# Kernel optimization log

Measured on AMD Instinct MI355X. Metric: run time of the kernel, lower is better.

Reference implementation:

```python
import jax, jax.numpy as jnp
import numpy as np
from functools import partial

N = 50000      # nodes
E = 800000     # edges
B = 64         # graphs in batch
D = 64         # embedding_dim (= per-head out_dim)
H = 2          # num_heads
G = 50         # n_gaussians
HID = 128      # hidden_dim of edge-filter net
MLP_DIM = 128  # mlp_dim of OutputMLP
OUT = 1        # output_dim
L = 3          # n_interactions
CUTOFF = 8.0
MEAN = 0.0
STD = 1.0


def ssp(x):
    # shifted softplus: softplus(x) - log(2)
    return jax.nn.softplus(x) - jnp.log(2.0)


def setup_inputs() -> dict:
    key = jax.random.key(0)
    ks = jax.random.split(key, 24)
    R = jax.random.normal(ks[0], (N, 3), dtype=jnp.float32) * 3.0
    Z = jax.random.randint(ks[1], (N,), 0, 100)
    src = jax.random.randint(ks[2], (E,), 0, N)
    dst = jax.random.randint(ks[3], (E,), 0, N)
    graph_ids = jnp.sort(jax.random.randint(ks[4], (N,), 0, B))
    # embedding table with padding_idx=0 zeroed
    emb_table = (jax.random.normal(ks[5], (100, D), dtype=jnp.float32) * 0.1).at[0].set(0.0)
    offsets = jnp.linspace(0.0, CUTOFF, G, dtype=jnp.float32)
    widths = jnp.full((G,), offsets[1] - offsets[0], dtype=jnp.float32)
    s = 0.1
    rn = lambda k, shp: jax.random.normal(k, shp, dtype=jnp.float32) * s
    return {
        "R": R, "Z": Z, "src": src, "dst": dst, "graph_ids": graph_ids,
        "emb_table": emb_table, "offsets": offsets, "widths": widths,
        "fc_w": rn(ks[6], (L, D, H * D)),
        "attn_l": rn(ks[7], (L, H, D)),
        "attn_r": rn(ks[8], (L, H, D)),
        "filt_w1": rn(ks[9], (L, G, HID)), "filt_b1": jnp.zeros((L, HID), jnp.float32),
        "filt_w2": rn(ks[10], (L, HID, H * D)), "filt_b2": jnp.zeros((L, H * D), jnp.float32),
        "mlp_w1": rn(ks[11], (L, H * D, D)), "mlp_b1": jnp.zeros((L, D), jnp.float32),
        "mlp_w2": rn(ks[12], (L, D, D)), "mlp_b2": jnp.zeros((L, D), jnp.float32),
        "out_w1": rn(ks[13], (D, MLP_DIM)), "out_b1": jnp.zeros((MLP_DIM,), jnp.float32),
        "out_w2": rn(ks[14], (MLP_DIM, OUT)), "out_b2": jnp.zeros((OUT,), jnp.float32),
    }


def _forward(R, emb_table, offsets, widths, fc_w, attn_l, attn_r,
             filt_w1, filt_b1, filt_w2, filt_b2,
             mlp_w1, mlp_b1, mlp_w2, mlp_b2,
             out_w1, out_b1, out_w2, out_b2,
             Z, src, dst, graph_ids):
    # per-edge distances
    r = jnp.linalg.norm(R[src] - R[dst], axis=1)  # (E,)
    # Gaussian smearing (trainable offsets/widths, schnetpack style)
    coeff = -0.5 / (widths ** 2)
    gs = jnp.exp(coeff * (r[:, None] - offsets) ** 2)  # (E, G)
    # cosine cutoff
    C = 0.5 * (jnp.cos(r * (jnp.pi / CUTOFF)) + 1.0) * (r < CUTOFF).astype(r.dtype)  # (E,)
    x = emb_table[Z]  # (N, D)
    for l in range(L):
        h = (x @ fc_w[l]).reshape(N, H, D)  # (N, H, D)
        # cfconv-style edge filter from gaussian features
        w = ssp(gs @ filt_w1[l] + filt_b1[l]) @ filt_w2[l] + filt_b2[l]  # (E, H*D)
        w = w.reshape(E, H, D)
        msg = h[src] * w * C[:, None, None]  # (E, H, D)
        # GAT attention, softmax over incoming edges per dst node
        el = jnp.einsum('nhd,hd->nh', h, attn_l[l])
        er = jnp.einsum('nhd,hd->nh', h, attn_r[l])
        e = jax.nn.leaky_relu(el[src] + er[dst], negative_slope=0.2)  # (E, H)
        m = jax.ops.segment_max(e, dst, num_segments=N)  # (N, H)
        ex = jnp.exp(e - m[dst])
        denom = jax.ops.segment_sum(ex, dst, num_segments=N)  # (N, H)
        alpha = ex / denom[dst]  # (E, H)
        agg = jax.ops.segment_sum(alpha[:, :, None] * msg, dst, num_segments=N)  # (N, H, D)
        v = ssp(agg).reshape(N, H * D)
        v = ssp(v @ mlp_w1[l] + mlp_b1[l]) @ mlp_w2[l] + mlp_b2[l]  # (N, D)
        x = x + v
    hh = ssp(x @ out_w1 + out_b1) @ out_w2 + out_b2  # (N, OUT)
    hh = hh * STD + MEAN
    return jax.ops.segment_sum(hh, graph_ids, num_segments=B)  # (B, OUT)


def reference(R, Z, src, dst, graph_ids, emb_table, offsets, widths,
              fc_w, attn_l, attn_r, filt_w1, filt_b1, filt_w2, filt_b2,
              mlp_w1, mlp_b1, mlp_w2, mlp_b2,
              out_w1, out_b1, out_w2, out_b2):
    return _forward(R, emb_table, offsets, widths, fc_w, attn_l, attn_r,
                    filt_w1, filt_b1, filt_w2, filt_b2,
                    mlp_w1, mlp_b1, mlp_w2, mlp_b2,
                    out_w1, out_b1, out_w2, out_b2,
                    Z, src, dst, graph_ids)
```

## Files before the change

### kernel.cpp

```cpp
#include <hip/hip_runtime.h>
#include <stdint.h>

#define N_NODES 50000
#define N_EDGES 800000
#define B_GRAPHS 64
#define D_DIM 64
#define HD 128
#define G_GAUSS 50
#define HID_DIM 128
#define L_LAYERS 3
#define LN2 0.69314718055994530942f
#define PI_OVER_8 0.39269908169872414f
#define NCHUNK 196

#define TN 64
#define TLD 132
#define XLD 68
#define NBLK ((N_NODES + TN - 1) / TN)

#define LUT_T 2048
#define LUT_ROWS (LUT_T + 1)
#define LROWS 8

__device__ __forceinline__ float sspf(float x) {
    float ax = fabsf(x);
    return fmaxf(x, 0.f) + __logf(1.f + __expf(-ax)) - LN2;
}
__device__ __forceinline__ unsigned short f2bf(float f) {
    union { float f; unsigned int i; } v; v.f = f;
    unsigned int u = v.i;
    return (unsigned short)((u + 0x7FFFu + ((u >> 16) & 1u)) >> 16);
}

__global__ void repr_prep(int* __restrict__ count, float* __restrict__ dout) {
    int i = blockIdx.x * 256 + threadIdx.x;
    if (i < N_NODES) count[i] = 0;
    else if (i < N_NODES + B_GRAPHS) dout[i - N_NODES] = 0.f;
}

#define NSUB (N_EDGES / 64)
#define ZB_T (2 * N_NODES / 4 + 2 * NSUB * 32)
__global__ void repr_zero_b(const int2* __restrict__ surv,
                            float* __restrict__ agg, float* __restrict__ denom) {
    int i = blockIdx.x * 256 + threadIdx.x;
    float4 z = make_float4(0.f, 0.f, 0.f, 0.f);
    if (i < 2 * N_NODES / 4) {
        ((float4*)denom)[i] = z;
    } else {
        int j = i - 2 * N_NODES / 4;
        if (j >= 2 * NSUB * 32) return;
        int row = j >> 5, c4 = j & 31;
        int sr = row >> 1;
        int p = sr * 64 + ((row & 1) ? 63 : 0);
        int d = (int)((unsigned)surv[p].x >> 16);
        *(float4*)&agg[(size_t)d * HD + c4 * 4] = z;
    }
}

__global__ __launch_bounds__(256) void repr_lut_build(
    const float* __restrict__ offs, const float* __restrict__ widths,
    const float* __restrict__ fw1, const float* __restrict__ fb1,
    const float* __restrict__ fw2, const float* __restrict__ fb2,
    unsigned int* __restrict__ lut)
{
    __shared__ float gs_s[LROWS + 1][G_GAUSS];
    __shared__ float hid_s[LROWS + 1][HID_DIM];
    __shared__ float wc_s[LROWS + 1][HD];
    const int nb = LUT_T / LROWS;
    int l = blockIdx.x / nb;
    int i0r = (blockIdx.x % nb) * LROWS;
    int tid = threadIdx.x;
    const float step = 8.0f / LUT_T;

    for (int j = tid; j < (LROWS + 1) * G_GAUSS; j += 256) {
        int r = j / G_GAUSS, k = j - r * G_GAUSS;
        float rr = (i0r + r) * step;
        float wdt = widths[k];
        float dr = rr - offs[k];
        gs_s[r][k] = expf(-0.5f / (wdt * wdt) * dr * dr);
    }
    __syncthreads();

    int c = tid & 127, sub = tid >> 7;
    int rlo = sub * 4;
    {
        const float* W1 = fw1 + (size_t)l * G_GAUSS * HID_DIM + c;
        float acc[5];
        float bb = fb1[l * HID_DIM + c];
        #pragma unroll
        for (int r = 0; r < 5; r++) acc[r] = bb;
        for (int k = 0; k < G_GAUSS; k++) {
            float wv = W1[k * HID_DIM];
            #pragma unroll
            for (int r = 0; r < 5; r++)
                acc[r] = fmaf(gs_s[rlo + r][k], wv, acc[r]);
        }
        #pragma unroll
        for (int r = 0; r < 5; r++) hid_s[rlo + r][c] = sspf(acc[r]);
    }
    __syncthreads();
    {
        const float* W2 = fw2 + (size_t)l * HID_DIM * HD + c;
        float acc[5];
        float bb = fb2[l * HD + c];
        #pragma unroll
        for (int r = 0; r < 5; r++) acc[r] = bb;
        for (int k = 0; k < HID_DIM; k++) {
            float wv = W2[k * HD];
            #pragma unroll
            for (int r = 0; r < 5; r++)
                acc[r] = fmaf(hid_s[rlo + r][k], wv, acc[r]);
        }
        #pragma unroll
        for (int r = 0; r < 5; r++) {
            float rr = (i0r + rlo + r) * step;
            float C = (rr < 8.0f) ? 0.5f * (cosf(rr * PI_OVER_8) + 1.f) : 0.f;
            wc_s[rlo + r][c] = acc[r] * C;
        }
    }
    __syncthreads();
    for (int j = tid; j < LROWS * HD; j += 256) {
        int r = j >> 7, cc = j & 127;
        unsigned int lo = f2bf(wc_s[r][cc]);
        unsigned int hi = f2bf(wc_s[r + 1][cc]);
        lut[((size_t)l * LUT_ROWS + i0r + r) * HD + cc] = lo | (hi << 16);
    }
    if (i0r == LUT_T - LROWS && tid < HD)
        lut[((size_t)l * LUT_ROWS + LUT_T) * HD + tid] = 0u;
}

__global__ void repr_hist(const float* __restrict__ R,
                          const int* __restrict__ src, const int* __restrict__ dst,
                          int* __restrict__ count,
                          int2* __restrict__ pk, unsigned short* __restrict__ rank) {
    int e = blockIdx.x * blockDim.x + threadIdx.x;
    if (e >= N_EDGES) return;
    int s = src[e], d = dst[e];
    float dx = R[3*s+0] - R[3*d+0];
    float dy = R[3*s+1] - R[3*d+1];
    float dz = R[3*s+2] - R[3*d+2];
    float r = sqrtf(dx*dx + dy*dy + dz*dz);
    unsigned rf = (r < 8.0f) ? (unsigned)(r * 16777216.f) : (2048u << 16);
    if (rf > (2048u << 16)) rf = 2048u << 16;
    pk[e] = make_int2((int)((unsigned)s | ((unsigned)d << 16)), (int)rf);
    int rnk = atomicAdd(&count[d], 1);
    rank[e] = (unsigned short)rnk;
}

__global__ void repr_scanA(const int* __restrict__ cnt, int* __restrict__ excl,
                           int* __restrict__ bsum) {
    __shared__ int tmp[256];
    int t = threadIdx.x, b = blockIdx.x;
    int i = b * 256 + t;
    int v = (i < N_NODES) ? cnt[i] : 0;
    tmp[t] = v; __syncthreads();
    for (int off = 1; off < 256; off <<= 1) {
        int add = (t >= off) ? tmp[t - off] : 0;
        __syncthreads();
        tmp[t] += add;
        __syncthreads();
    }
    if (i < N_NODES) excl[i] = tmp[t] - v;
    if (t == 255) bsum[b] = tmp[255];
}
__global__ void repr_scanB(const int* __restrict__ bsum, int* __restrict__ bpref) {
    __shared__ int tmp[256];
    int t = threadIdx.x;
    int v = (t < NCHUNK) ? bsum[t] : 0;
    tmp[t] = v; __syncthreads();
    for (int off = 1; off < 256; off <<= 1) {
        int add = (t >= off) ? tmp[t - off] : 0;
        __syncthreads();
        tmp[t] += add;
        __syncthreads();
    }
    if (t < NCHUNK) bpref[t] = tmp[t] - v;
}
__global__ void repr_scanC(const int* __restrict__ excl, const int* __restrict__ bpref,
                           int* __restrict__ rowptr) {
    int i = blockIdx.x * 256 + threadIdx.x;
    if (i < N_NODES) rowptr[i] = excl[i] + bpref[blockIdx.x];
}

__global__ void repr_scatter(const int2* __restrict__ pk,
                             const unsigned short* __restrict__ rank,
                             const int* __restrict__ rowptr,
                             int2* __restrict__ surv) {
    int e = blockIdx.x * blockDim.x + threadIdx.x;
    if (e >= N_EDGES) return;
    int2 v = pk[e];
    int d = (int)((unsigned)v.x >> 16);
    surv[rowptr[d] + (int)rank[e]] = v;
}


__device__ __forceinline__ void load_ssp_agg(int base, int tid,
        const float* __restrict__ agg, const float* __restrict__ denom,
        float* __restrict__ bufA) {
    int row = tid >> 2;
    int c0 = (tid & 3) << 5;
    int n = base + row;
    float2 dn = *(const float2*)&denom[2 * (size_t)n];
    float i0v = dn.x > 0.f ? 1.f / dn.x : 0.f;
    float i1v = dn.y > 0.f ? 1.f / dn.y : 0.f;
    float inv = (c0 < 64) ? i0v : i1v;
    const float* ap = agg + (size_t)n * HD + c0;
    float* tp = bufA + row * TLD + c0;
    #pragma unroll
    for (int j = 0; j < 8; j++) {
        float4 v = *(const float4*)(ap + j * 4);
        tp[j*4+0] = sspf(v.x * inv); tp[j*4+1] = sspf(v.y * inv);
        tp[j*4+2] = sspf(v.z * inv); tp[j*4+3] = sspf(v.w * inv);
    }
}

__device__ __forceinline__ void gemm_mlp(int base, int tid,
        const float* __restrict__ w1, const float* __restrict__ b1,
        const float* __restrict__ w2, const float* __restrict__ b2,
        float* __restrict__ x, float* __restrict__ bufA, float* __restrict__ v1s)
{
    const int rg = tid >> 4, cg = tid & 15;
    const int r0 = rg * 4, c0 = cg * 4;
    float acc[4][4];
    #pragma unroll
    for (int r = 0; r < 4; r++)
        #pragma unroll
        for (int c = 0; c < 4; c++) acc[r][c] = 0.f;
    for (int k0 = 0; k0 < 128; k0 += 4) {
        float av[4][4];
        #pragma unroll
        for (int r = 0; r < 4; r++)
            *(float4*)av[r] = *(const float4*)&bufA[(r0 + r) * TLD + k0];
        #pragma unroll
        for (int kk = 0; kk < 4; kk++) {
            float4 wv = *(const float4*)(w1 + (k0 + kk) * 64 + c0);
            float wf[4] = {wv.x, wv.y, wv.z, wv.w};
            #pragma unroll
            for (int r = 0; r < 4; r++)
                #pragma unroll
                for (int c = 0; c < 4; c++)
                    acc[r][c] = fmaf(av[r][kk], wf[c], acc[r][c]);
        }
    }
    {
        float4 bv = *(const float4*)(b1 + c0);
        float ba[4] = {bv.x, bv.y, bv.z, bv.w};
        #pragma unroll
        for (int r = 0; r < 4; r++)
            #pragma unroll
            for (int c = 0; c < 4; c++)
                v1s[(r0 + r) * XLD + c0 + c] = sspf(acc[r][c] + ba[c]);
    }
    __syncthreads();
    float acc2[4][4];
    #pragma unroll
    for (int r = 0; r < 4; r++)
        #pragma unroll
        for (int c = 0; c < 4; c++) acc2[r][c] = 0.f;
    for (int k0 = 0; k0 < 64; k0 += 4) {
        float av[4][4];
        #pragma unroll
        for (int r = 0; r < 4; r++)
            *(float4*)av[r] = *(const float4*)&v1s[(r0 + r) * XLD + k0];
        #pragma unroll
        for (int kk = 0; kk < 4; kk++) {
            float4 wv = *(const float4*)(w2 + (k0 + kk) * 64 + c0);
            float wf[4] = {wv.x, wv.y, wv.z, wv.w};
            #pragma unroll
            for (int r = 0; r < 4; r++)
                #pragma unroll
                for (int c = 0; c < 4; c++)
                    acc2[r][c] = fmaf(av[r][kk], wf[c], acc2[r][c]);
        }
    }
    {
        float4 bv = *(const float4*)(b2 + c0);
        #pragma unroll
        for (int r = 0; r < 4; r++) {
            int n = base + r0 + r;
            float4 xv = *(const float4*)(x + (size_t)n * 64 + c0);
            float4 o;
            o.x = acc2[r][0] + bv.x + xv.x;
            o.y = acc2[r][1] + bv.y + xv.y;
            o.z = acc2[r][2] + bv.z + xv.z;
            o.w = acc2[r][3] + bv.w + xv.w;
            *(float4*)&bufA[(r0 + r) * XLD + c0] = o;
            if (n < N_NODES) *(float4*)(x + (size_t)n * 64 + c0) = o;
        }
    }
    __syncthreads();
}

__device__ __forceinline__ void gemm_h(int base, int tid,
        const float* __restrict__ bufA,
        const float* __restrict__ fc_w, const float* __restrict__ attn_l,
        const float* __restrict__ attn_r,
        unsigned int* __restrict__ hq, float* __restrict__ el, float* __restrict__ er)
{
    const int rg = tid >> 4, cg = tid & 15;
    const int r0 = rg * 4, c0 = cg * 8;
    float acc[4][8];
    #pragma unroll
    for (int r = 0; r < 4; r++)
        #pragma unroll
        for (int c = 0; c < 8; c++) acc[r][c] = 0.f;
    for (int k0 = 0; k0 < 64; k0 += 4) {
        float av[4][4];
        #pragma unroll
        for (int r = 0; r < 4; r++)
            *(float4*)av[r] = *(const float4*)&bufA[(r0 + r) * XLD + k0];
        #pragma unroll
        for (int kk = 0; kk < 4; kk++) {
            float4 w0 = *(const float4*)(fc_w + (k0 + kk) * 128 + c0);
            float4 w1v = *(const float4*)(fc_w + (k0 + kk) * 128 + c0 + 4);
            float wf[8] = {w0.x, w0.y, w0.z, w0.w, w1v.x, w1v.y, w1v.z, w1v.w};
            #pragma unroll
            for (int r = 0; r < 4; r++)
                #pragma unroll
                for (int c = 0; c < 8; c++)
                    acc[r][c] = fmaf(av[r][kk], wf[c], acc[r][c]);
        }
    }
    float al[8], ar[8];
    #pragma unroll
    for (int c = 0; c < 8; c++) { al[c] = attn_l[c0 + c]; ar[c] = attn_r[c0 + c]; }
    int head = cg >> 3;
    #pragma unroll
    for (int r = 0; r < 4; r++) {
        int n = base + r0 + r;
        float pel = 0.f, per = 0.f;
        #pragma unroll
        for (int c = 0; c < 8; c++) {
            pel = fmaf(acc[r][c], al[c], pel);
            per = fmaf(acc[r][c], ar[c], per);
        }
        if (n < N_NODES) {
            uint4 pv;
            pv.x = (unsigned int)f2bf(acc[r][0]) | ((unsigned int)f2bf(acc[r][1]) << 16);
            pv.y = (unsigned int)f2bf(acc[r][2]) | ((unsigned int)f2bf(acc[r][3]) << 16);
            pv.z = (unsigned int)f2bf(acc[r][4]) | ((unsigned int)f2bf(acc[r][5]) << 16);
            pv.w = (unsigned int)f2bf(acc[r][6]) | ((unsigned int)f2bf(acc[r][7]) << 16);
            *(uint4*)(hq + (size_t)n * 64 + cg * 4) = pv;
        }
        #pragma unroll
        for (int off = 1; off < 8; off <<= 1) {
            pel += __shfl_xor(pel, off, 64);
            per += __shfl_xor(per, off, 64);
        }
        if ((cg & 7) == 0 && n < N_NODES) {
            el[n * 2 + head] = pel;
            er[n * 2 + head] = per;
        }
    }
}

__global__ __launch_bounds__(256) void repr_embed_h(
        const float* __restrict__ emb, const int* __restrict__ Z,
        const float* __restrict__ fc_w, const float* __restrict__ attn_l,
        const float* __restrict__ attn_r,
        float* __restrict__ x, unsigned int* __restrict__ hq,
        float* __restrict__ el, float* __restrict__ er) {
    __shared__ float bufA[TN * XLD];
    int base = blockIdx.x * TN, tid = threadIdx.x;
    int row = tid >> 2;
    int c0 = (tid & 3) << 4;
    int n = base + row;
    int z = (n < N_NODES) ? Z[n] : 0;
    const float* ep = emb + (size_t)z * D_DIM + c0;
    float* bp = bufA + row * XLD + c0;
    #pragma unroll
    for (int j = 0; j < 4; j++) {
        float4 v = *(const float4*)(ep + j * 4);
        *(float4*)(bp + j * 4) = v;
        if (n < N_NODES) *(float4*)(x + (size_t)n * D_DIM + c0 + j * 4) = v;
    }
    __syncthreads();
    gemm_h(base, tid, bufA, fc_w, attn_l, attn_r, hq, el, er);
}

__global__ __launch_bounds__(256) void repr_mlp_h(
        const float* __restrict__ agg, const float* __restrict__ denom,
        const float* __restrict__ w1, const float* __restrict__ b1,
        const float* __restrict__ w2, const float* __restrict__ b2,
        const float* __restrict__ fc_w, const float* __restrict__ attn_l,
        const float* __restrict__ attn_r,
        float* __restrict__ x, unsigned int* __restrict__ hq,
        float* __restrict__ el, float* __restrict__ er) {
    __shared__ float bufA[TN * TLD];
    __shared__ float v1s[TN * XLD];
    int base = blockIdx.x * TN, tid = threadIdx.x;
    load_ssp_agg(base, tid, agg, denom, bufA);
    __syncthreads();
    gemm_mlp(base, tid, w1, b1, w2, b2, x, bufA, v1s);
    gemm_h(base, tid, bufA, fc_w, attn_l, attn_r, hq, el, er);
}

__global__ __launch_bounds__(256) void repr_mlp_out(
        const float* __restrict__ agg, const float* __restrict__ denom,
        const float* __restrict__ w1, const float* __restrict__ b1,
        const float* __restrict__ w2, const float* __restrict__ b2,
        const float* __restrict__ ow1, const float* __restrict__ ob1,
        const float* __restrict__ ow2, const float* __restrict__ ob2,
        float* __restrict__ x, float* __restrict__ hh) {
    __shared__ float bufA[TN * TLD];
    __shared__ float v1s[TN * XLD];
    int base = blockIdx.x * TN, tid = threadIdx.x;
    load_ssp_agg(base, tid, agg, denom, bufA);
    __syncthreads();
    gemm_mlp(base, tid, w1, b1, w2, b2, x, bufA, v1s);
    const int rg = tid >> 4, cg = tid & 15;
    const int r0 = rg * 4, c0 = cg * 8;
    float acc[4][8];
    #pragma unroll
    for (int r = 0; r < 4; r++)
        #pragma unroll
        for (int c = 0; c < 8; c++) acc[r][c] = 0.f;
    for (int k0 = 0; k0 < 64; k0 += 4) {
        float av[4][4];
        #pragma unroll
        for (int r = 0; r < 4; r++)
            *(float4*)av[r] = *(const float4*)&bufA[(r0 + r) * XLD + k0];
        #pragma unroll
        for (int kk = 0; kk < 4; kk++) {
            float4 w0 = *(const float4*)(ow1 + (k0 + kk) * 128 + c0);
            float4 w1v = *(const float4*)(ow1 + (k0 + kk) * 128 + c0 + 4);
            float wf[8] = {w0.x, w0.y, w0.z, w0.w, w1v.x, w1v.y, w1v.z, w1v.w};
            #pragma unroll
            for (int r = 0; r < 4; r++)
                #pragma unroll
                for (int c = 0; c < 8; c++)
                    acc[r][c] = fmaf(av[r][kk], wf[c], acc[r][c]);
        }
    }
    float o1[8], w2c[8];
    #pragma unroll
    for (int c = 0; c < 8; c++) { o1[c] = ob1[c0 + c]; w2c[c] = ow2[c0 + c]; }
    #pragma unroll
    for (int r = 0; r < 4; r++) {
        int n = base + r0 + r;
        float s = 0.f;
        #pragma unroll
        for (int c = 0; c < 8; c++)
            s = fmaf(sspf(acc[r][c] + o1[c]), w2c[c], s);
        #pragma unroll
        for (int off = 1; off < 16; off <<= 1)
            s += __shfl_xor(s, off, 64);
        if (cg == 0 && n < N_NODES) hh[n] = s + ob2[0];
    }
}

#define TILE 256
__global__ __launch_bounds__(256) void repr_msg_lut(
    const int2* __restrict__ surv,
    const float* __restrict__ el, const float* __restrict__ er,
    const unsigned int* __restrict__ hq,
    const unsigned int* __restrict__ lut,
    float* __restrict__ agg, float* __restrict__ denom)
{
    __shared__ int4 rowinfo[TILE];
    __shared__ float scl[TILE][2];
    int base = blockIdx.x * TILE;
    int tid = threadIdx.x;
    int d_own; float e0, e1;
    {
        int2 ev = surv[base + tid];
        int sn = (int)((unsigned)ev.x & 0xFFFFu);
        d_own  = (int)((unsigned)ev.x >> 16);
        unsigned rf = (unsigned)ev.y;
        int i0 = (int)(rf >> 16);
        float fr = (float)(rf & 0xFFFFu) * (1.f / 65536.f);
        float2 a = *(const float2*)&el[2 * sn];
        float2 b = *(const float2*)&er[2 * d_own];
        float v0 = a.x + b.x; v0 = v0 >= 0.f ? v0 : 0.2f * v0;
        float v1 = a.y + b.y; v1 = v1 >= 0.f ? v1 : 0.2f * v1;
        e0 = __expf(v0); e1 = __expf(v1);
        rowinfo[tid] = make_int4(i0, sn, d_own, __float_as_int(fr));
        scl[tid][0] = e0; scl[tid][1] = e1;
    }
    __syncthreads();
    {
        bool headl = (tid == 0) || (rowinfo[tid - 1].z != d_own);
        if (headl) {
            float s0 = e0, s1 = e1;
            for (int r = tid + 1; r < TILE; r++) {
                if (rowinfo[r].z != d_own) break;
                s0 += scl[r][0]; s1 += scl[r][1];
            }
            atomicAdd(&denom[2 * d_own], s0);
            atomicAdd(&denom[2 * d_own + 1], s1);
        }
    }
    const int cp = tid & 63;
    const int sp = tid >> 6;
    const int head = cp >> 5;
    const int lo = sp * 64;
    const uint2* __restrict__ l2p = (const uint2*)lut;
    float sum0 = 0.f, sum1 = 0.f;
    int cur_d = -1;
    int seg_first = 1;
    #pragma unroll 4
    for (int j = 0; j < 64; j++) {
        int r = lo + j;
        int4 ri = rowinfo[r];
        if (ri.z != cur_d) {
            if (cur_d >= 0) {
                float* ap = &agg[(size_t)cur_d * HD + 2 * cp];
                if (seg_first) { atomicAdd(ap, sum0); atomicAdd(ap + 1, sum1); }
                else *(float2*)ap = make_float2(sum0, sum1);
            }
            cur_d = ri.z; sum0 = 0.f; sum1 = 0.f; seg_first = (j == 0);
        }
        uint2 tv = l2p[(size_t)ri.x * 64 + cp];
        float fr = __int_as_float(ri.w);
        float wa0 = __uint_as_float(tv.x << 16);
        float wa1 = __uint_as_float(tv.x & 0xFFFF0000u);
        float wb0 = __uint_as_float(tv.y << 16);
        float wb1 = __uint_as_float(tv.y & 0xFFFF0000u);
        unsigned int hv = hq[(size_t)ri.y * 64 + cp];
        float ha = __uint_as_float(hv << 16);
        float hb = __uint_as_float(hv & 0xFFFF0000u);
        float s = scl[r][head];
        float wa = fmaf(fr, wa1 - wa0, wa0);
        float wb = fmaf(fr, wb1 - wb0, wb0);
        sum0 = fmaf(wa * ha, s, sum0);
        sum1 = fmaf(wb * hb, s, sum1);
    }
    if (cur_d >= 0) {
        float* ap = &agg[(size_t)cur_d * HD + 2 * cp];
        atomicAdd(ap, sum0); atomicAdd(ap + 1, sum1);
    }
}

__global__ void repr_gsum(const float* __restrict__ hh, const int* __restrict__ gids,
                          float* __restrict__ dout) {
    __shared__ float bins[B_GRAPHS];
    int t = threadIdx.x;
    if (t < B_GRAPHS) bins[t] = 0.f;
    __syncthreads();
    int i = blockIdx.x * 256 + t;
    if (i < N_NODES) atomicAdd(&bins[gids[i]], hh[i]);
    __syncthreads();
    if (t < B_GRAPHS && bins[t] != 0.f) atomicAdd(&dout[t], bins[t]);
}

extern "C" void kernel_launch(void* const* d_in, const int* in_sizes, int n_in,
                              void* d_out, int out_size, void* d_ws, size_t ws_size,
                              hipStream_t stream) {
    (void)in_sizes; (void)n_in; (void)out_size; (void)ws_size;
    const float* R      = (const float*)d_in[0];
    const int*   Z      = (const int*)d_in[1];
    const int*   src    = (const int*)d_in[2];
    const int*   dst    = (const int*)d_in[3];
    const int*   gids   = (const int*)d_in[4];
    const float* emb    = (const float*)d_in[5];
    const float* offs   = (const float*)d_in[6];
    const float* widths = (const float*)d_in[7];
    const float* fc_w   = (const float*)d_in[8];
    const float* attn_l = (const float*)d_in[9];
    const float* attn_r = (const float*)d_in[10];
    const float* fw1    = (const float*)d_in[11];
    const float* fb1    = (const float*)d_in[12];
    const float* fw2    = (const float*)d_in[13];
    const float* fb2    = (const float*)d_in[14];
    const float* mw1    = (const float*)d_in[15];
    const float* mb1    = (const float*)d_in[16];
    const float* mw2    = (const float*)d_in[17];
    const float* mb2    = (const float*)d_in[18];
    const float* ow1    = (const float*)d_in[19];
    const float* ob1    = (const float*)d_in[20];
    const float* ow2    = (const float*)d_in[21];
    const float* ob2    = (const float*)d_in[22];

    char* p = (char*)d_ws;
    float* x      = (float*)p; p += (size_t)N_NODES * 64 * 4;
    unsigned int* hq = (unsigned int*)p; p += (size_t)N_NODES * 64 * 4;
    float* el     = (float*)p; p += (size_t)N_NODES * 2 * 4;
    float* er     = (float*)p; p += (size_t)N_NODES * 2 * 4;
    float* denom  = (float*)p; p += (size_t)N_NODES * 2 * 4;
    float* agg    = (float*)p; p += (size_t)N_NODES * 128 * 4;
    int2*  surv   = (int2*)p;  p += (size_t)N_EDGES * 8;
    int2*  pk     = (int2*)p;  p += (size_t)N_EDGES * 8;
    float* hh     = (float*)p; p += (size_t)N_NODES * 4;
    int*   bsum   = (int*)p;   p += 1024;
    int*   bpref  = (int*)p;   p += 1024;
    unsigned int* lut = (unsigned int*)pk;
    int* count = (int*)x;
    int* excl  = (int*)((char*)x + 256 * 1024);
    unsigned short* rank = (unsigned short*)((char*)x + 512 * 1024);
    int* rowptr = (int*)((char*)x + 2560 * 1024);

    repr_prep<<<(N_NODES + B_GRAPHS + 255) / 256, 256, 0, stream>>>(
        count, (float*)d_out);
    repr_hist<<<N_EDGES / 256, 256, 0, stream>>>(R, src, dst, count, pk, rank);
    repr_scanA<<<NCHUNK, 256, 0, stream>>>(count, excl, bsum);
    repr_scanB<<<1, 256, 0, stream>>>(bsum, bpref);
    repr_scanC<<<NCHUNK, 256, 0, stream>>>(excl, bpref, rowptr);
    repr_scatter<<<N_EDGES / 256, 256, 0, stream>>>(pk, rank, rowptr, surv);

    repr_lut_build<<<L_LAYERS * (LUT_T / LROWS), 256, 0, stream>>>(
        offs, widths, fw1, fb1, fw2, fb2, lut);

    repr_embed_h<<<NBLK, 256, 0, stream>>>(
        emb, Z, fc_w, attn_l, attn_r, x, hq, el, er);

    for (int l = 0; l < L_LAYERS; l++) {
        repr_zero_b<<<(ZB_T + 255) / 256, 256, 0, stream>>>(surv, agg, denom);
        repr_msg_lut<<<N_EDGES / TILE, 256, 0, stream>>>(
            surv, el, er, hq, lut + (size_t)l * LUT_ROWS * HD, agg, denom);
        if (l < L_LAYERS - 1) {
            repr_mlp_h<<<NBLK, 256, 0, stream>>>(
                agg, denom, mw1 + (size_t)l * 128 * 64, mb1 + l * 64,
                mw2 + (size_t)l * 64 * 64, mb2 + l * 64,
                fc_w + (size_t)(l + 1) * 64 * 128, attn_l + (l + 1) * 128,
                attn_r + (l + 1) * 128, x, hq, el, er);
        } else {
            repr_mlp_out<<<NBLK, 256, 0, stream>>>(
                agg, denom, mw1 + (size_t)l * 128 * 64, mb1 + l * 64,
                mw2 + (size_t)l * 64 * 64, mb2 + l * 64,
                ow1, ob1, ow2, ob2, x, hh);
        }
    }
    repr_gsum<<<NCHUNK, 256, 0, stream>>>(hh, gids, (float*)d_out);
}
```

Before: 576.4 us.

## Move distance packing into scatter and process two edge rows per thread in message kernel

The histogram kernel now only counts destinations and assigns ranks, while the scatter kernel computes the distance and packed edge record directly, so the intermediate pk buffer no longer has to be written and read back. The LUT gets its own workspace region instead of aliasing pk. The message kernel tile grows to 512 edges per 256-thread block, and each thread handles two independent 64-row segment streams that it interleaves. This gives more memory-level parallelism and fewer blocks. The cost is more registers, more shared memory per block, and an extra partial-tile guard.

```diff
diff --git a/kernel.cpp b/kernel.cpp
--- a/kernel.cpp
+++ b/kernel.cpp
@@ -129,22 +129,12 @@
         lut[((size_t)l * LUT_ROWS + LUT_T) * HD + tid] = 0u;
 }
 
-__global__ void repr_hist(const float* __restrict__ R,
-                          const int* __restrict__ src, const int* __restrict__ dst,
+__global__ void repr_hist(const int* __restrict__ dst,
                           int* __restrict__ count,
-                          int2* __restrict__ pk, unsigned short* __restrict__ rank) {
+                          unsigned short* __restrict__ rank) {
     int e = blockIdx.x * blockDim.x + threadIdx.x;
     if (e >= N_EDGES) return;
-    int s = src[e], d = dst[e];
-    float dx = R[3*s+0] - R[3*d+0];
-    float dy = R[3*s+1] - R[3*d+1];
-    float dz = R[3*s+2] - R[3*d+2];
-    float r = sqrtf(dx*dx + dy*dy + dz*dz);
-    unsigned rf = (r < 8.0f) ? (unsigned)(r * 16777216.f) : (2048u << 16);
-    if (rf > (2048u << 16)) rf = 2048u << 16;
-    pk[e] = make_int2((int)((unsigned)s | ((unsigned)d << 16)), (int)rf);
-    int rnk = atomicAdd(&count[d], 1);
-    rank[e] = (unsigned short)rnk;
+    rank[e] = (unsigned short)atomicAdd(&count[dst[e]], 1);
 }
 
 __global__ void repr_scanA(const int* __restrict__ cnt, int* __restrict__ excl,
@@ -182,15 +172,22 @@
     if (i < N_NODES) rowptr[i] = excl[i] + bpref[blockIdx.x];
 }
 
-__global__ void repr_scatter(const int2* __restrict__ pk,
+__global__ void repr_scatter(const float* __restrict__ R,
+                             const int* __restrict__ src, const int* __restrict__ dst,
                              const unsigned short* __restrict__ rank,
                              const int* __restrict__ rowptr,
                              int2* __restrict__ surv) {
     int e = blockIdx.x * blockDim.x + threadIdx.x;
     if (e >= N_EDGES) return;
-    int2 v = pk[e];
-    int d = (int)((unsigned)v.x >> 16);
-    surv[rowptr[d] + (int)rank[e]] = v;
+    int s = src[e], d = dst[e];
+    float dx = R[3*s+0] - R[3*d+0];
+    float dy = R[3*s+1] - R[3*d+1];
+    float dz = R[3*s+2] - R[3*d+2];
+    float r = sqrtf(dx*dx + dy*dy + dz*dz);
+    unsigned rf = (r < 8.0f) ? (unsigned)(r * 16777216.f) : (2048u << 16);
+    if (rf > (2048u << 16)) rf = 2048u << 16;
+    surv[rowptr[d] + (int)rank[e]] =
+        make_int2((int)((unsigned)s | ((unsigned)d << 16)), (int)rf);
 }
 
 
@@ -449,7 +446,7 @@
     }
 }
 
-#define TILE 256
+#define TILE 512
 __global__ __launch_bounds__(256) void repr_msg_lut(
     const int2* __restrict__ surv,
     const float* __restrict__ el, const float* __restrict__ er,
@@ -460,74 +457,107 @@
     __shared__ int4 rowinfo[TILE];
     __shared__ float scl[TILE][2];
     int base = blockIdx.x * TILE;
+    int nc = N_EDGES - base; if (nc > TILE) nc = TILE;
     int tid = threadIdx.x;
-    int d_own; float e0, e1;
-    {
-        int2 ev = surv[base + tid];
+    for (int j = tid; j < nc; j += 256) {
+        int2 ev = surv[base + j];
         int sn = (int)((unsigned)ev.x & 0xFFFFu);
-        d_own  = (int)((unsigned)ev.x >> 16);
+        int d  = (int)((unsigned)ev.x >> 16);
         unsigned rf = (unsigned)ev.y;
         int i0 = (int)(rf >> 16);
         float fr = (float)(rf & 0xFFFFu) * (1.f / 65536.f);
         float2 a = *(const float2*)&el[2 * sn];
-        float2 b = *(const float2*)&er[2 * d_own];
+        float2 b = *(const float2*)&er[2 * d];
         float v0 = a.x + b.x; v0 = v0 >= 0.f ? v0 : 0.2f * v0;
         float v1 = a.y + b.y; v1 = v1 >= 0.f ? v1 : 0.2f * v1;
-        e0 = __expf(v0); e1 = __expf(v1);
-        rowinfo[tid] = make_int4(i0, sn, d_own, __float_as_int(fr));
-        scl[tid][0] = e0; scl[tid][1] = e1;
-    }
-    __syncthreads();
-    {
-        bool headl = (tid == 0) || (rowinfo[tid - 1].z != d_own);
+        rowinfo[j] = make_int4(i0, sn, d, __float_as_int(fr));
+        scl[j][0] = __expf(v0); scl[j][1] = __expf(v1);
+    }
+    __syncthreads();
+    for (int j = tid; j < nc; j += 256) {
+        int dj = rowinfo[j].z;
+        bool headl = (j == 0) || (rowinfo[j - 1].z != dj);
         if (headl) {
-            float s0 = e0, s1 = e1;
-            for (int r = tid + 1; r < TILE; r++) {
-                if (rowinfo[r].z != d_own) break;
+            float s0 = scl[j][0], s1 = scl[j][1];
+            for (int r = j + 1; r < nc && rowinfo[r].z == dj; r++) {
                 s0 += scl[r][0]; s1 += scl[r][1];
             }
-            atomicAdd(&denom[2 * d_own], s0);
-            atomicAdd(&denom[2 * d_own + 1], s1);
+            atomicAdd(&denom[2 * dj], s0);
+            atomicAdd(&denom[2 * dj + 1], s1);
         }
     }
     const int cp = tid & 63;
     const int sp = tid >> 6;
     const int head = cp >> 5;
-    const int lo = sp * 64;
+    const int loA = sp * 64;
+    const int loB = (sp + 4) * 64;
+    const bool hasB = loB < nc;
     const uint2* __restrict__ l2p = (const uint2*)lut;
-    float sum0 = 0.f, sum1 = 0.f;
-    int cur_d = -1;
-    int seg_first = 1;
-    #pragma unroll 4
+    float a0 = 0.f, a1 = 0.f, b0 = 0.f, b1 = 0.f;
+    int curA = -1, curB = -1;
+    int fsA = 1, fsB = 1;
+    #pragma unroll 2
     for (int j = 0; j < 64; j++) {
-        int r = lo + j;
-        int4 ri = rowinfo[r];
-        if (ri.z != cur_d) {
-            if (cur_d >= 0) {
-                float* ap = &agg[(size_t)cur_d * HD + 2 * cp];
-                if (seg_first) { atomicAdd(ap, sum0); atomicAdd(ap + 1, sum1); }
-                else *(float2*)ap = make_float2(sum0, sum1);
+        {
+            int r = loA + j;
+            int4 ri = rowinfo[r];
+            if (ri.z != curA) {
+                if (curA >= 0) {
+                    float* ap = &agg[(size_t)curA * HD + 2 * cp];
+                    if (fsA) { atomicAdd(ap, a0); atomicAdd(ap + 1, a1); }
+                    else *(float2*)ap = make_float2(a0, a1);
+                }
+                curA = ri.z; a0 = 0.f; a1 = 0.f; fsA = (j == 0);
             }
-            cur_d = ri.z; sum0 = 0.f; sum1 = 0.f; seg_first = (j == 0);
-        }
-        uint2 tv = l2p[(size_t)ri.x * 64 + cp];
-        float fr = __int_as_float(ri.w);
-        float wa0 = __uint_as_float(tv.x << 16);
-        float wa1 = __uint_as_float(tv.x & 0xFFFF0000u);
-        float wb0 = __uint_as_float(tv.y << 16);
-        float wb1 = __uint_as_float(tv.y & 0xFFFF0000u);
-        unsigned int hv = hq[(size_t)ri.y * 64 + cp];
-        float ha = __uint_as_float(hv << 16);
-        float hb = __uint_as_float(hv & 0xFFFF0000u);
-        float s = scl[r][head];
-        float wa = fmaf(fr, wa1 - wa0, wa0);
-        float wb = fmaf(fr, wb1 - wb0, wb0);
-        sum0 = fmaf(wa * ha, s, sum0);
-        sum1 = fmaf(wb * hb, s, sum1);
-    }
-    if (cur_d >= 0) {
-        float* ap = &agg[(size_t)cur_d * HD + 2 * cp];
-        atomicAdd(ap, sum0); atomicAdd(ap + 1, sum1);
+            uint2 tv = l2p[(size_t)ri.x * 64 + cp];
+            unsigned int hv = hq[(size_t)ri.y * 64 + cp];
+            float fr = __int_as_float(ri.w);
+            float s = scl[r][head];
+            float wa0 = __uint_as_float(tv.x << 16);
+            float wa1 = __uint_as_float(tv.x & 0xFFFF0000u);
+            float wb0 = __uint_as_float(tv.y << 16);
+            float wb1 = __uint_as_float(tv.y & 0xFFFF0000u);
+            float ha = __uint_as_float(hv << 16);
+            float hb = __uint_as_float(hv & 0xFFFF0000u);
+            float wa = fmaf(fr, wa1 - wa0, wa0);
+            float wb = fmaf(fr, wb1 - wb0, wb0);
+            a0 = fmaf(wa * ha, s, a0);
+            a1 = fmaf(wb * hb, s, a1);
+        }
+        if (hasB) {
+            int r = loB + j;
+            int4 ri = rowinfo[r];
+            if (ri.z != curB) {
+                if (curB >= 0) {
+                    float* ap = &agg[(size_t)curB * HD + 2 * cp];
+                    if (fsB) { atomicAdd(ap, b0); atomicAdd(ap + 1, b1); }
+                    else *(float2*)ap = make_float2(b0, b1);
+                }
+                curB = ri.z; b0 = 0.f; b1 = 0.f; fsB = (j == 0);
+            }
+            uint2 tv = l2p[(size_t)ri.x * 64 + cp];
+            unsigned int hv = hq[(size_t)ri.y * 64 + cp];
+            float fr = __int_as_float(ri.w);
+            float s = scl[r][head];
+            float wa0 = __uint_as_float(tv.x << 16);
+            float wa1 = __uint_as_float(tv.x & 0xFFFF0000u);
+            float wb0 = __uint_as_float(tv.y << 16);
+            float wb1 = __uint_as_float(tv.y & 0xFFFF0000u);
+            float ha = __uint_as_float(hv << 16);
+            float hb = __uint_as_float(hv & 0xFFFF0000u);
+            float wa = fmaf(fr, wa1 - wa0, wa0);
+            float wb = fmaf(fr, wb1 - wb0, wb0);
+            b0 = fmaf(wa * ha, s, b0);
+            b1 = fmaf(wb * hb, s, b1);
+        }
+    }
+    if (curA >= 0) {
+        float* ap = &agg[(size_t)curA * HD + 2 * cp];
+        atomicAdd(ap, a0); atomicAdd(ap + 1, a1);
+    }
+    if (hasB && curB >= 0) {
+        float* ap = &agg[(size_t)curB * HD + 2 * cp];
+        atomicAdd(ap, b0); atomicAdd(ap + 1, b1);
     }
 }
 
@@ -579,11 +609,10 @@
     float* denom  = (float*)p; p += (size_t)N_NODES * 2 * 4;
     float* agg    = (float*)p; p += (size_t)N_NODES * 128 * 4;
     int2*  surv   = (int2*)p;  p += (size_t)N_EDGES * 8;
-    int2*  pk     = (int2*)p;  p += (size_t)N_EDGES * 8;
+    unsigned int* lut = (unsigned int*)p; p += (size_t)L_LAYERS * LUT_ROWS * HD * 4;
     float* hh     = (float*)p; p += (size_t)N_NODES * 4;
     int*   bsum   = (int*)p;   p += 1024;
     int*   bpref  = (int*)p;   p += 1024;
-    unsigned int* lut = (unsigned int*)pk;
     int* count = (int*)x;
     int* excl  = (int*)((char*)x + 256 * 1024);
     unsigned short* rank = (unsigned short*)((char*)x + 512 * 1024);
@@ -591,11 +620,12 @@
 
     repr_prep<<<(N_NODES + B_GRAPHS + 255) / 256, 256, 0, stream>>>(
         count, (float*)d_out);
-    repr_hist<<<N_EDGES / 256, 256, 0, stream>>>(R, src, dst, count, pk, rank);
+    repr_hist<<<N_EDGES / 256, 256, 0, stream>>>(dst, count, rank);
     repr_scanA<<<NCHUNK, 256, 0, stream>>>(count, excl, bsum);
     repr_scanB<<<1, 256, 0, stream>>>(bsum, bpref);
     repr_scanC<<<NCHUNK, 256, 0, stream>>>(excl, bpref, rowptr);
-    repr_scatter<<<N_EDGES / 256, 256, 0, stream>>>(pk, rank, rowptr, surv);
+    repr_scatter<<<N_EDGES / 256, 256, 0, stream>>>(
+        R, src, dst, rank, rowptr, surv);
 
     repr_lut_build<<<L_LAYERS * (LUT_T / LROWS), 256, 0, stream>>>(
         offs, widths, fw1, fb1, fw2, fb2, lut);
@@ -605,7 +635,7 @@
 
     for (int l = 0; l < L_LAYERS; l++) {
         repr_zero_b<<<(ZB_T + 255) / 256, 256, 0, stream>>>(surv, agg, denom);
-        repr_msg_lut<<<N_EDGES / TILE, 256, 0, stream>>>(
+        repr_msg_lut<<<(N_EDGES + TILE - 1) / TILE, 256, 0, stream>>>(
             surv, el, er, hq, lut + (size_t)l * LUT_ROWS * HD, agg, denom);
         if (l < L_LAYERS - 1) {
             repr_mlp_h<<<NBLK, 256, 0, stream>>>(
```

New measurement: 555.5 us (median of 2 runs). 3.6% less time.
